# Kernel optimization log

Hardware: AMD Instinct MI355X
Metric: run time of the kernel (lower is better)

The kernel has to match this reference:

```python
import jax, jax.numpy as jnp
import numpy as np

VOCAB = 32000
EMB = 512
UNITS = 1024
B, T = 128, 256


def setup_inputs() -> dict:
    key = jax.random.key(0)
    ks = jax.random.split(key, 9)
    s = 0.05
    return {
        "tokens": jax.random.randint(ks[0], (B, T), 0, VOCAB),
        "emb_table": jax.random.normal(ks[1], (VOCAB, EMB), jnp.float32) * s,
        "Wx_f": jax.random.normal(ks[2], (EMB, 3 * UNITS), jnp.float32) * s,
        "Wh_f": jax.random.normal(ks[3], (UNITS, 3 * UNITS), jnp.float32) * s,
        "b_f": jnp.zeros((2, 3 * UNITS), jnp.float32),  # [input_bias, recurrent_bias] (reset_after=True)
        "Wx_b": jax.random.normal(ks[4], (EMB, 3 * UNITS), jnp.float32) * s,
        "Wh_b": jax.random.normal(ks[5], (UNITS, 3 * UNITS), jnp.float32) * s,
        "b_b": jnp.zeros((2, 3 * UNITS), jnp.float32),
        "fc_W": jax.random.normal(ks[6], (2 * UNITS, UNITS), jnp.float32) * s,
        "fc_b": jnp.zeros((UNITS,), jnp.float32),
    }


def _gru_dir(x_proj, mask, Wh, b_rec, reverse):
    # x_proj: [B,T,3U] precomputed input projections (z|r|h gate order, Keras),
    # mask: [B,T] bool. Keras GRU v2 semantics: reset_after=True,
    # sigmoid recurrent activation, tanh activation; masked steps carry state.
    b, u = x_proj.shape[0], Wh.shape[0]

    def step(h, inputs):
        xp, m = inputs  # [B,3U], [B]
        rec = h @ Wh + b_rec  # [B,3U]
        xz, xr, xh = jnp.split(xp, 3, axis=-1)
        rz, rr, rh = jnp.split(rec, 3, axis=-1)
        z = jax.nn.sigmoid(xz + rz)
        r = jax.nn.sigmoid(xr + rr)
        hh = jnp.tanh(xh + r * rh)
        h_new = z * h + (1.0 - z) * hh
        h_new = jnp.where(m[:, None], h_new, h)
        return h_new, h_new

    h0 = jnp.zeros((b, u), x_proj.dtype)
    xs = (jnp.swapaxes(x_proj, 0, 1), jnp.swapaxes(mask, 0, 1))  # time-major
    h_last, outs = jax.lax.scan(step, h0, xs, reverse=reverse)
    return jnp.swapaxes(outs, 0, 1), h_last  # [B,T,U], [B,U]


def reference(tokens, emb_table, Wx_f, Wh_f, b_f, Wx_b, Wh_b, b_b, fc_W, fc_b):
    mask = tokens != 0  # Embedding(mask_zero=True)
    x = emb_table[tokens]  # [B,T,E]
    xp_f = x @ Wx_f + b_f[0]
    xp_b = x @ Wx_b + b_b[0]
    out_f, h_f = _gru_dir(xp_f, mask, Wh_f, b_f[1], reverse=False)
    out_b, h_b = _gru_dir(xp_b, mask, Wh_b, b_b[1], reverse=True)
    output = jnp.concatenate([out_f, out_b], axis=-1)  # [B,T,2U]
    hidden = jnp.concatenate([h_f, h_b], axis=-1) @ fc_W + fc_b  # [B,U]
    return output, hidden
```

## Files before the change

### kernel.cpp

```cpp
#include <hip/hip_runtime.h>


#define T_SEQ 256
#define BATCH 128
#define EMB_D 512
#define UNITS 1024
#define NROWS (BATCH * T_SEQ)
#define N3U 3072
#define N6U 6144
#define XT_STRIDE 786432
#define HSTR (BATCH * 2048)
#define HROT 16

#define SBAR()      __builtin_amdgcn_s_barrier()
#define SCHED0()    __builtin_amdgcn_sched_barrier(0)
#define WAIT_LGKM() asm volatile("s_waitcnt lgkmcnt(0)" ::: "memory")
#define WAIT_VM()   asm volatile("s_waitcnt vmcnt(0)" ::: "memory")

typedef __attribute__((ext_vector_type(8))) __bf16 bfv8;
typedef __attribute__((ext_vector_type(4))) float f32x4;

__device__ inline unsigned short f2bf(float f) {
  union { float f; unsigned int u; } x; x.f = f;
  unsigned int u = x.u;
  unsigned int r = (u + 0x7fffu + ((u >> 16) & 1u)) >> 16;
  return (unsigned short)r;
}
__device__ inline float bf2f(unsigned short h) {
  union { unsigned int u; float f; } x; x.u = ((unsigned int)h) << 16;
  return x.f;
}
__device__ inline f32x4 mfma16(bfv8 a, bfv8 b, f32x4 c) {
  return __builtin_amdgcn_mfma_f32_16x16x32_bf16(a, b, c, 0, 0, 0);
}
__device__ inline void gl_lds16(const unsigned short* g, unsigned short* l) {
  __builtin_amdgcn_global_load_lds(
      (const __attribute__((address_space(1))) void*)g,
      (__attribute__((address_space(3))) void*)l, 16, 0, 0);
}

__global__ __launch_bounds__(256) void k_transpose(const float* __restrict__ src,
                                                   unsigned short* __restrict__ dst,
                                                   int K, int N) {
  __shared__ float tile[32][33];
  int k0 = blockIdx.x * 32, n0 = blockIdx.y * 32;
  int tx = threadIdx.x & 31, ty = threadIdx.x >> 5;
#pragma unroll
  for (int i = 0; i < 4; ++i)
    tile[ty + i * 8][tx] = src[(size_t)(k0 + ty + i * 8) * N + n0 + tx];
  __syncthreads();
#pragma unroll
  for (int i = 0; i < 4; ++i)
    dst[(size_t)(n0 + ty + i * 8) * K + k0 + tx] = f2bf(tile[tx][ty + i * 8]);
}

__global__ __launch_bounds__(256) void k_gather(const int* __restrict__ tokens,
                                                const float* __restrict__ emb,
                                                unsigned short* __restrict__ Xbf) {
  int idx = blockIdx.x * 256 + threadIdx.x;
  int row = idx >> 7;
  int c4 = (idx & 127) * 4;
  int tok = tokens[row];
  float4 v = *(const float4*)(emb + (size_t)tok * EMB_D + c4);
  ushort4 p;
  p.x = f2bf(v.x); p.y = f2bf(v.y); p.z = f2bf(v.z); p.w = f2bf(v.w);
  *(ushort4*)(Xbf + (size_t)row * EMB_D + c4) = p;
}

__global__ __launch_bounds__(256) void k_bias(const float* __restrict__ bf_,
                                              const float* __restrict__ bb_,
                                              float* __restrict__ biasX,
                                              float* __restrict__ biasH) {
  int i = blockIdx.x * 256 + threadIdx.x;
  if (i >= N6U) return;
  if (i < N3U) { biasX[i] = bf_[i];        biasH[i] = bf_[N3U + i]; }
  else         { biasX[i] = bb_[i - N3U];  biasH[i] = bb_[i]; }
}

__global__ __launch_bounds__(256) void k_tokt(const int* __restrict__ tokens,
                                              int* __restrict__ tokT) {
  int i = blockIdx.x * 256 + threadIdx.x;
  int b = i >> 8, t = i & 255;
  tokT[t * BATCH + b] = tokens[i];
}

__global__ __launch_bounds__(256) void k_gemm(const unsigned short* __restrict__ A,
                                              const unsigned short* __restrict__ BT,
                                              const float* __restrict__ bias,
                                              void* __restrict__ C,
                                              int M, int N, int K, int mode) {
  __shared__ unsigned short As[128 * 32];
  __shared__ unsigned short Bs[128 * 32];
  const int mt = blockIdx.x, nt = blockIdx.y;
  const int tid = threadIdx.x;
  const int wid = tid >> 6, lane = tid & 63;
  const int wm = (wid >> 1) * 64, wn = (wid & 1) * 64;
  const int l15 = lane & 15, lk = (lane >> 4) * 8;

  f32x4 acc[4][4];
#pragma unroll
  for (int i = 0; i < 4; ++i)
#pragma unroll
    for (int j = 0; j < 4; ++j) acc[i][j] = (f32x4){0.f, 0.f, 0.f, 0.f};

  const int r = tid >> 2;
  const int cc = (tid & 3) * 8;
  const unsigned short* ga0 = A + (size_t)(mt * 128 + r) * K + cc;
  const unsigned short* ga1 = ga0 + (size_t)64 * K;
  const unsigned short* gb0 = BT + (size_t)(nt * 128 + r) * K + cc;
  const unsigned short* gb1 = gb0 + (size_t)64 * K;
  unsigned short* lA0 = As + r * 32 + cc;
  unsigned short* lA1 = As + (64 + r) * 32 + cc;
  unsigned short* lB0 = Bs + r * 32 + cc;
  unsigned short* lB1 = Bs + (64 + r) * 32 + cc;

  for (int k0 = 0; k0 < K; k0 += 32) {
    __syncthreads();
    gl_lds16(ga0 + k0, lA0);
    gl_lds16(ga1 + k0, lA1);
    gl_lds16(gb0 + k0, lB0);
    gl_lds16(gb1 + k0, lB1);
    __syncthreads();
    bfv8 af[4], bfr[4];
#pragma unroll
    for (int i = 0; i < 4; ++i) {
      af[i]  = *(const bfv8*)(As + (wm + i * 16 + l15) * 32 + lk);
      bfr[i] = *(const bfv8*)(Bs + (wn + i * 16 + l15) * 32 + lk);
    }
#pragma unroll
    for (int i = 0; i < 4; ++i)
#pragma unroll
      for (int j = 0; j < 4; ++j) acc[i][j] = mfma16(af[i], bfr[j], acc[i][j]);
  }

#pragma unroll
  for (int j = 0; j < 4; ++j) {
    const int col = nt * 128 + wn + j * 16 + l15;
    const float bv = bias[col];
    const int dirc = (col >= N3U) ? 1 : 0;
    const int cm = col - dirc * N3U;
    const int g = cm >> 10;
    const int uu = cm & 1023;
    const size_t cbase = (size_t)dirc * 393216 + (size_t)(uu >> 4) * 6144 +
                         (size_t)g * 16 + (uu & 15);
#pragma unroll
    for (int i = 0; i < 4; ++i) {
      const int row0 = mt * 128 + wm + i * 16 + (lane >> 4) * 4;
#pragma unroll
      for (int q = 0; q < 4; ++q) {
        const float v = acc[i][j][q] + bv;
        const int row = row0 + q;
        if (mode == 1) {
          ((float*)C)[(size_t)row * N + col] = v;
        } else {
          const int b = row >> 8, tt = row & 255;
          ((unsigned short*)C)[(size_t)tt * XT_STRIDE + cbase + (size_t)b * 48] = f2bf(v);
        }
      }
    }
  }
}

__global__ __launch_bounds__(512) void k_scan(const unsigned short* __restrict__ XPn,
                                              const unsigned short* __restrict__ WhT,
                                              const float* __restrict__ biasH,
                                              const int* __restrict__ tokT,
                                              unsigned short* __restrict__ hbR,
                                              float* __restrict__ out,
                                              unsigned int* __restrict__ bar) {
  __shared__ unsigned short Wl[3 * 128 * 16 * 8];
  __shared__ unsigned short xb[64 * 48];
  __shared__ int tkb[64];
  __shared__ unsigned short bounce[64 * 24];
  __shared__ float red[4][64][13];

  const int bid = blockIdx.x;
  const int grp = bid & 3;
  const int dir = grp >> 1;
  const int mg  = grp & 1;
  const int ut  = bid >> 2;
  const int u0 = ut * 16, m0 = mg * 64;
  const int sub = ut & 7;
  const int tid = threadIdx.x;

  for (int c = tid; c < 6144; c += 512) {
    const int g  = c >> 11;
    const int kb = (c >> 4) & 127;
    const int uu = c & 15;
    *(uint4*)(Wl + (((g << 7) | kb) * 16 + uu) * 8) =
        *(const uint4*)(WhT + (((size_t)(dir * N3U + (g << 10) + u0 + uu)) << 10) + (kb << 3));
  }

  const int lane = tid & 63, wid = tid >> 6;
  const int wlo = wid & 3, kh = wid >> 2;
  const int l15 = lane & 15, hi = lane >> 4;
  const size_t aoff = ((size_t)(m0 + wlo * 16 + l15) << 11) + (dir << 10) + (kh << 9) + (hi << 3);
  const int u = u0 + l15;
  const float bz  = biasH[dir * N3U + u];
  const float brg = biasH[dir * N3U + 1024 + u];
  const float bhg = biasH[dir * N3U + 2048 + u];
  const int rb = wlo * 16 + (hi << 2);
  const int ob = m0 + rb;
  const size_t woff = (dir << 10) + u;
  const int sr = tid >> 2, sc4 = (tid & 3) << 2;
  const size_t soff = ((size_t)(m0 + sr) << 11) + (dir << 10) + u0 + sc4;

  const unsigned short* xpb = XPn + (size_t)dir * 393216 + (size_t)ut * 6144 + (size_t)m0 * 48;

  unsigned long long pf0, pf1 = 0; int pft = 0;
  {
    const int t0 = dir ? (T_SEQ - 1) : 0;
    const unsigned long long* xs = (const unsigned long long*)(xpb + (size_t)t0 * XT_STRIDE);
    pf0 = xs[tid];
    if (tid < 256) pf1 = xs[tid + 512];
    if (tid < 64) pft = tokT[t0 * BATCH + m0 + tid];
  }

  float hreg[4] = {0.f, 0.f, 0.f, 0.f};
  float oreg[4];
  __syncthreads();

  for (int s = 0; s < T_SEQ; ++s) {
    const int t = dir ? (T_SEQ - 1 - s) : s;
    const unsigned short* hrd = hbR + (size_t)((s + HROT - 1) & (HROT - 1)) * HSTR;
    unsigned short* hwr       = hbR + (size_t)(s & (HROT - 1)) * HSTR;

    {
      unsigned long long* xd = (unsigned long long*)xb;
      xd[tid] = pf0;
      if (tid < 256) xd[tid + 512] = pf1;
      if (tid < 64) tkb[tid] = pft;
    }
    WAIT_LGKM(); SCHED0(); SBAR(); SCHED0();

    float xz[4], xr[4], xh[4]; int tok[4];
    if (kh == 0) {
#pragma unroll
      for (int q = 0; q < 4; ++q) {
        const int xo = (rb + q) * 48 + l15;
        xz[q] = bf2f(xb[xo]);
        xr[q] = bf2f(xb[xo + 16]);
        xh[q] = bf2f(xb[xo + 32]);
        tok[q] = tkb[rb + q];
      }
    }

    if (s + 1 < T_SEQ) {
      const int tn = dir ? (T_SEQ - 2 - s) : (s + 1);
      const unsigned long long* xs = (const unsigned long long*)(xpb + (size_t)tn * XT_STRIDE);
      pf0 = xs[tid];
      if (tid < 256) pf1 = xs[tid + 512];
      if (tid < 64) pft = tokT[tn * BATCH + m0 + tid];
    }

    const unsigned short* ap = hrd + aoff;
    f32x4 az0 = {0.f,0.f,0.f,0.f}, az1 = az0, ar0 = az0, ar1 = az0, ah0 = az0, ah1 = az0;
#pragma unroll
    for (int ks = 0; ks < 8; ++ks) {
      bfv8 a0 = *(const bfv8*)(ap + (ks << 6));
      bfv8 a1 = *(const bfv8*)(ap + (ks << 6) + 32);
      const unsigned short* wp = Wl + ((((kh << 6) + (ks << 3) + hi) * 16 + l15) * 8);
      bfv8 wz0 = *(const bfv8*)(wp);
      bfv8 wr0 = *(const bfv8*)(wp + (1 << 14));
      bfv8 wh0 = *(const bfv8*)(wp + (2 << 14));
      bfv8 wz1 = *(const bfv8*)(wp + 512);
      bfv8 wr1 = *(const bfv8*)(wp + (1 << 14) + 512);
      bfv8 wh1 = *(const bfv8*)(wp + (2 << 14) + 512);
      az0 = mfma16(a0, wz0, az0); ar0 = mfma16(a0, wr0, ar0); ah0 = mfma16(a0, wh0, ah0);
      az1 = mfma16(a1, wz1, az1); ar1 = mfma16(a1, wr1, ar1); ah1 = mfma16(a1, wh1, ah1);
    }
    f32x4 az = az0 + az1, ar = ar0 + ar1, ah = ah0 + ah1;

    if (kh == 1) {
#pragma unroll
      for (int j = 0; j < 4; ++j) {
        red[wlo][lane][j]     = az[j];
        red[wlo][lane][4 + j] = ar[j];
        red[wlo][lane][8 + j] = ah[j];
      }
    }
    WAIT_LGKM(); SCHED0(); SBAR(); SCHED0();

    if (kh == 0) {
#pragma unroll
      for (int j = 0; j < 4; ++j) {
        az[j] += red[wlo][lane][j];
        ar[j] += red[wlo][lane][4 + j];
        ah[j] += red[wlo][lane][8 + j];
      }
#pragma unroll
      for (int q = 0; q < 4; ++q) {
        const float z  = 1.f / (1.f + __expf(-(xz[q] + az[q] + bz)));
        const float r  = 1.f / (1.f + __expf(-(xr[q] + ar[q] + brg)));
        const float hh = tanhf(xh[q] + r * (ah[q] + bhg));
        float hn = z * hreg[q] + (1.f - z) * hh;
        if (tok[q] == 0) hn = hreg[q];
        hreg[q] = hn;
        oreg[q] = hn;
        bounce[(rb + q) * 24 + l15] = f2bf(hn);
      }
    }

    WAIT_LGKM(); SCHED0(); SBAR(); SCHED0();
    if (tid < 256) {
      unsigned long long v = *(const unsigned long long*)(bounce + sr * 24 + sc4);
      __hip_atomic_store((unsigned long long*)(hwr + soff), v,
                         __ATOMIC_RELAXED, __HIP_MEMORY_SCOPE_AGENT);
    }

    if (s + 1 < T_SEQ) {
      WAIT_VM(); SCHED0(); SBAR(); SCHED0();
      if (kh == 0) {
#pragma unroll
        for (int q = 0; q < 4; ++q)
          out[((size_t)((ob + q) * T_SEQ + t) << 11) + woff] = oreg[q];
      }
      if (tid == 0)
        __hip_atomic_fetch_add(&bar[((grp << 3) | sub) << 6], 1u,
                               __ATOMIC_RELAXED, __HIP_MEMORY_SCOPE_AGENT);
      if (tid < 8) {
        const unsigned tgt = 8u * (unsigned)(s + 1);
        unsigned int* p = &bar[((grp << 3) | tid) << 6];
        while (__hip_atomic_load(p, __ATOMIC_RELAXED, __HIP_MEMORY_SCOPE_AGENT) < tgt)
          __builtin_amdgcn_s_sleep(2);
        if ((s & (HROT - 1)) == HROT - 1)
          __builtin_amdgcn_fence(__ATOMIC_ACQUIRE, "agent");
      }
      SBAR(); SCHED0();
    } else {
      if (kh == 0) {
#pragma unroll
        for (int q = 0; q < 4; ++q)
          out[((size_t)((ob + q) * T_SEQ + t) << 11) + woff] = oreg[q];
      }
    }
  }
}

extern "C" void kernel_launch(void* const* d_in, const int* in_sizes, int n_in,
                              void* d_out, int out_size, void* d_ws, size_t ws_size,
                              hipStream_t stream) {
  const int* tokens = (const int*)d_in[0];
  const float* emb  = (const float*)d_in[1];
  const float* Wx_f = (const float*)d_in[2];
  const float* Wh_f = (const float*)d_in[3];
  const float* b_f  = (const float*)d_in[4];
  const float* Wx_b = (const float*)d_in[5];
  const float* Wh_b = (const float*)d_in[6];
  const float* b_b  = (const float*)d_in[7];
  const float* fc_W = (const float*)d_in[8];
  const float* fc_b = (const float*)d_in[9];
  float* out = (float*)d_out;

  char* w = (char*)d_ws;
  unsigned short* XPn = (unsigned short*)w; w += (size_t)NROWS * N6U * 2;
  unsigned short* Xbf = (unsigned short*)w; w += (size_t)NROWS * EMB_D * 2;
  unsigned short* WxT = (unsigned short*)w; w += (size_t)N6U * EMB_D * 2;
  unsigned short* WhT = (unsigned short*)w; w += (size_t)N6U * UNITS * 2;
  unsigned short* fcWT = (unsigned short*)w; w += (size_t)UNITS * 2048 * 2;
  unsigned short* hbR = (unsigned short*)w; w += (size_t)HROT * HSTR * 2;
  float* biasX = (float*)w; w += N6U * 4;
  float* biasH = (float*)w; w += N6U * 4;
  int* tokT = (int*)w; w += NROWS * 4;
  unsigned int* bar = (unsigned int*)w; w += 2048 * sizeof(unsigned int);

  (void)hipMemsetAsync((void*)(hbR + (size_t)(HROT - 1) * HSTR), 0, (size_t)HSTR * 2, stream);
  (void)hipMemsetAsync((void*)bar, 0, 2048 * sizeof(unsigned int), stream);

  k_transpose<<<dim3(EMB_D / 32, N3U / 32), 256, 0, stream>>>(Wx_f, WxT, EMB_D, N3U);
  k_transpose<<<dim3(EMB_D / 32, N3U / 32), 256, 0, stream>>>(Wx_b, WxT + (size_t)N3U * EMB_D, EMB_D, N3U);
  k_transpose<<<dim3(UNITS / 32, N3U / 32), 256, 0, stream>>>(Wh_f, WhT, UNITS, N3U);
  k_transpose<<<dim3(UNITS / 32, N3U / 32), 256, 0, stream>>>(Wh_b, WhT + (size_t)N3U * UNITS, UNITS, N3U);
  k_transpose<<<dim3(2048 / 32, 1024 / 32), 256, 0, stream>>>(fc_W, fcWT, 2048, 1024);
  k_bias<<<24, 256, 0, stream>>>(b_f, b_b, biasX, biasH);
  k_tokt<<<NROWS / 256, 256, 0, stream>>>(tokens, tokT);
  k_gather<<<(NROWS * 128) / 256, 256, 0, stream>>>(tokens, emb, Xbf);

  k_gemm<<<dim3(NROWS / 128, N6U / 128), 256, 0, stream>>>(Xbf, WxT, biasX, XPn, NROWS, N6U, EMB_D, 0);

  k_scan<<<256, 512, 0, stream>>>(XPn, WhT, biasH, tokT, hbR, out, bar);

  k_gemm<<<dim3(1, 8), 256, 0, stream>>>(hbR + (size_t)(HROT - 1) * HSTR, fcWT, fc_b,
                                         out + (size_t)NROWS * 2048, BATCH, UNITS, 2048, 1);
}
```

Measured before the change: 2.459 ms.

## Replace block-level step barrier with per-wave flags and direct h stores

Each kh==0 wave now writes its bf16 hidden values straight to the global ring buffer with atomic stores, then bumps its own flag. Previously each block bounced the values through LDS, did a coalesced 64-bit store, and then passed several block barriers. Waves poll all 32 producer flags at the start of the next step. The x-projection and token staging moves from LDS into per-lane register prefetch issued after the MFMA loop, and the reduction buffer is double-buffered to drop the trailing barrier. This removes several s_barriers per timestep, at the cost of scattered 16-bit global stores and more polling traffic.

After: 3.451 ms. +40.4%, slower.

```diff
diff --git a/kernel.cpp b/kernel.cpp
--- a/kernel.cpp
+++ b/kernel.cpp
@@ -169,10 +169,7 @@
                                               float* __restrict__ out,
                                               unsigned int* __restrict__ bar) {
   __shared__ unsigned short Wl[3 * 128 * 16 * 8];
-  __shared__ unsigned short xb[64 * 48];
-  __shared__ int tkb[64];
-  __shared__ unsigned short bounce[64 * 24];
-  __shared__ float red[4][64][13];
+  __shared__ float red[2][4][64][13];
 
   const int bid = blockIdx.x;
   const int grp = bid & 3;
@@ -180,7 +177,6 @@
   const int mg  = grp & 1;
   const int ut  = bid >> 2;
   const int u0 = ut * 16, m0 = mg * 64;
-  const int sub = ut & 7;
   const int tid = threadIdx.x;
 
   for (int c = tid; c < 6144; c += 512) {
@@ -202,22 +198,24 @@
   const int rb = wlo * 16 + (hi << 2);
   const int ob = m0 + rb;
   const size_t woff = (dir << 10) + u;
-  const int sr = tid >> 2, sc4 = (tid & 3) << 2;
-  const size_t soff = ((size_t)(m0 + sr) << 11) + (dir << 10) + u0 + sc4;
+
+  unsigned int* myflag = &bar[((grp << 5) | ((ut & 7) << 2) | wid) << 4];
 
   const unsigned short* xpb = XPn + (size_t)dir * 393216 + (size_t)ut * 6144 + (size_t)m0 * 48;
 
-  unsigned long long pf0, pf1 = 0; int pft = 0;
-  {
+  unsigned short px[12]; int4 ptok = {0, 0, 0, 0};
+  if (kh == 0) {
     const int t0 = dir ? (T_SEQ - 1) : 0;
-    const unsigned long long* xs = (const unsigned long long*)(xpb + (size_t)t0 * XT_STRIDE);
-    pf0 = xs[tid];
-    if (tid < 256) pf1 = xs[tid + 512];
-    if (tid < 64) pft = tokT[t0 * BATCH + m0 + tid];
+    const unsigned short* xs = xpb + (size_t)t0 * XT_STRIDE;
+#pragma unroll
+    for (int q = 0; q < 4; ++q)
+#pragma unroll
+      for (int g = 0; g < 3; ++g)
+        px[q * 3 + g] = xs[(rb + q) * 48 + g * 16 + l15];
+    ptok = *(const int4*)(tokT + t0 * BATCH + ob);
   }
 
   float hreg[4] = {0.f, 0.f, 0.f, 0.f};
-  float oreg[4];
   __syncthreads();
 
   for (int s = 0; s < T_SEQ; ++s) {
@@ -225,32 +223,19 @@
     const unsigned short* hrd = hbR + (size_t)((s + HROT - 1) & (HROT - 1)) * HSTR;
     unsigned short* hwr       = hbR + (size_t)(s & (HROT - 1)) * HSTR;
 
-    {
-      unsigned long long* xd = (unsigned long long*)xb;
-      xd[tid] = pf0;
-      if (tid < 256) xd[tid + 512] = pf1;
-      if (tid < 64) tkb[tid] = pft;
-    }
-    WAIT_LGKM(); SCHED0(); SBAR(); SCHED0();
-
-    float xz[4], xr[4], xh[4]; int tok[4];
-    if (kh == 0) {
-#pragma unroll
-      for (int q = 0; q < 4; ++q) {
-        const int xo = (rb + q) * 48 + l15;
-        xz[q] = bf2f(xb[xo]);
-        xr[q] = bf2f(xb[xo + 16]);
-        xh[q] = bf2f(xb[xo + 32]);
-        tok[q] = tkb[rb + q];
-      }
-    }
-
-    if (s + 1 < T_SEQ) {
-      const int tn = dir ? (T_SEQ - 2 - s) : (s + 1);
-      const unsigned long long* xs = (const unsigned long long*)(xpb + (size_t)tn * XT_STRIDE);
-      pf0 = xs[tid];
-      if (tid < 256) pf1 = xs[tid + 512];
-      if (tid < 64) pft = tokT[tn * BATCH + m0 + tid];
+    if (s > 0) {
+      if (lane < 32) {
+        const unsigned tgt = 8u * (unsigned)s;
+        unsigned int* p = &bar[((grp << 5) | lane) << 4];
+        while (__hip_atomic_load(p, __ATOMIC_RELAXED, __HIP_MEMORY_SCOPE_AGENT) < tgt)
+          __builtin_amdgcn_s_sleep(2);
+      }
+      SCHED0();
+      if ((s & (HROT - 1)) == 0) {
+        SBAR(); SCHED0();
+        if (wid == 0) __builtin_amdgcn_fence(__ATOMIC_ACQUIRE, "agent");
+        SCHED0(); SBAR(); SCHED0();
+      }
     }
 
     const unsigned short* ap = hrd + aoff;
@@ -271,12 +256,33 @@
     }
     f32x4 az = az0 + az1, ar = ar0 + ar1, ah = ah0 + ah1;
 
+    float xz[4], xr[4], xh[4]; int tok[4];
+    if (kh == 0) {
+#pragma unroll
+      for (int q = 0; q < 4; ++q) {
+        xz[q] = bf2f(px[q * 3 + 0]);
+        xr[q] = bf2f(px[q * 3 + 1]);
+        xh[q] = bf2f(px[q * 3 + 2]);
+      }
+      tok[0] = ptok.x; tok[1] = ptok.y; tok[2] = ptok.z; tok[3] = ptok.w;
+      if (s + 1 < T_SEQ) {
+        const int tn = dir ? (T_SEQ - 2 - s) : (s + 1);
+        const unsigned short* xs = xpb + (size_t)tn * XT_STRIDE;
+#pragma unroll
+        for (int q = 0; q < 4; ++q)
+#pragma unroll
+          for (int g = 0; g < 3; ++g)
+            px[q * 3 + g] = xs[(rb + q) * 48 + g * 16 + l15];
+        ptok = *(const int4*)(tokT + tn * BATCH + ob);
+      }
+    }
+
     if (kh == 1) {
 #pragma unroll
       for (int j = 0; j < 4; ++j) {
-        red[wlo][lane][j]     = az[j];
-        red[wlo][lane][4 + j] = ar[j];
-        red[wlo][lane][8 + j] = ah[j];
+        red[s & 1][wlo][lane][j]     = az[j];
+        red[s & 1][wlo][lane][4 + j] = ar[j];
+        red[s & 1][wlo][lane][8 + j] = ah[j];
       }
     }
     WAIT_LGKM(); SCHED0(); SBAR(); SCHED0();
@@ -284,9 +290,9 @@
     if (kh == 0) {
 #pragma unroll
       for (int j = 0; j < 4; ++j) {
-        az[j] += red[wlo][lane][j];
-        ar[j] += red[wlo][lane][4 + j];
-        ah[j] += red[wlo][lane][8 + j];
+        az[j] += red[s & 1][wlo][lane][j];
+        ar[j] += red[s & 1][wlo][lane][4 + j];
+        ah[j] += red[s & 1][wlo][lane][8 + j];
       }
 #pragma unroll
       for (int q = 0; q < 4; ++q) {
@@ -296,42 +302,14 @@
         float hn = z * hreg[q] + (1.f - z) * hh;
         if (tok[q] == 0) hn = hreg[q];
         hreg[q] = hn;
-        oreg[q] = hn;
-        bounce[(rb + q) * 24 + l15] = f2bf(hn);
-      }
-    }
-
-    WAIT_LGKM(); SCHED0(); SBAR(); SCHED0();
-    if (tid < 256) {
-      unsigned long long v = *(const unsigned long long*)(bounce + sr * 24 + sc4);
-      __hip_atomic_store((unsigned long long*)(hwr + soff), v,
-                         __ATOMIC_RELAXED, __HIP_MEMORY_SCOPE_AGENT);
-    }
-
-    if (s + 1 < T_SEQ) {
-      WAIT_VM(); SCHED0(); SBAR(); SCHED0();
-      if (kh == 0) {
-#pragma unroll
-        for (int q = 0; q < 4; ++q)
-          out[((size_t)((ob + q) * T_SEQ + t) << 11) + woff] = oreg[q];
-      }
-      if (tid == 0)
-        __hip_atomic_fetch_add(&bar[((grp << 3) | sub) << 6], 1u,
-                               __ATOMIC_RELAXED, __HIP_MEMORY_SCOPE_AGENT);
-      if (tid < 8) {
-        const unsigned tgt = 8u * (unsigned)(s + 1);
-        unsigned int* p = &bar[((grp << 3) | tid) << 6];
-        while (__hip_atomic_load(p, __ATOMIC_RELAXED, __HIP_MEMORY_SCOPE_AGENT) < tgt)
-          __builtin_amdgcn_s_sleep(2);
-        if ((s & (HROT - 1)) == HROT - 1)
-          __builtin_amdgcn_fence(__ATOMIC_ACQUIRE, "agent");
-      }
-      SBAR(); SCHED0();
-    } else {
-      if (kh == 0) {
-#pragma unroll
-        for (int q = 0; q < 4; ++q)
-          out[((size_t)((ob + q) * T_SEQ + t) << 11) + woff] = oreg[q];
+        __hip_atomic_store(hwr + ((size_t)(ob + q) << 11) + woff, f2bf(hn),
+                           __ATOMIC_RELAXED, __HIP_MEMORY_SCOPE_AGENT);
+        out[((size_t)((ob + q) * T_SEQ + t) << 11) + woff] = hn;
+      }
+      if (s + 1 < T_SEQ) {
+        WAIT_VM(); SCHED0();
+        if (lane == 0)
+          __hip_atomic_fetch_add(myflag, 1u, __ATOMIC_RELAXED, __HIP_MEMORY_SCOPE_AGENT);
       }
     }
   }
```
